# Kernel optimization log

Hardware: AMD Instinct MI355X
Metric: run time of the kernel (lower is better)

Reference implementation:

```python
import jax, jax.numpy as jnp
import numpy as np

S = 128           # inp_spatial_size
B = 4             # batch (4th coord column)
N = 200000        # active voxels
PLANES = (4, 8, 16, 32)   # feat_aug_mode='power', m=4
LEAK = 0.01
EPS = 1e-4        # sparseconvnet BatchNorm default eps
NOUT = 64


def _conv(x, w, stride, pad):
    return jax.lax.conv_general_dilated(
        x, w, (stride,) * 3, pad,
        dimension_numbers=('NCDHW', 'OIDHW', 'NCDHW'))


def _bn_lrelu(x, mask, g, b):
    # SCN BatchNormLeakyReLU: stats over ACTIVE sites only (x is zero at inactive)
    cnt = jnp.maximum(jnp.sum(mask), 1.0)
    mean = jnp.sum(x, axis=(0, 2, 3, 4)) / cnt
    var = jnp.sum(x * x, axis=(0, 2, 3, 4)) / cnt - mean * mean
    sc = (g * jax.lax.rsqrt(var + EPS))[None, :, None, None, None]
    y = (x - mean[None, :, None, None, None]) * sc + b[None, :, None, None, None]
    y = jnp.where(y >= 0, y, LEAK * y)
    return y * mask


def _pool2(x, red):
    b, c, d, h, w = x.shape
    return red(x.reshape(b, c, d // 2, 2, h // 2, 2, w // 2, 2), axis=(3, 5, 7))


def _forward(point_cloud, w0, g1, b1, wc1, g2, b2, wc2, g3, b3, wc3, wlin, blin):
    ci = point_cloud[:, :3].astype(jnp.int32)
    bi = point_cloud[:, 3].astype(jnp.int32)
    f = point_cloud[:, 4]
    # InputLayer mode=3: sum features of duplicate coordinates
    dense = jnp.zeros((B, 1, S, S, S), jnp.float32).at[bi, 0, ci[:, 0], ci[:, 1], ci[:, 2]].add(f)
    mask = jnp.zeros((B, 1, S, S, S), jnp.float32).at[bi, 0, ci[:, 0], ci[:, 1], ci[:, 2]].set(1.0)
    # SubmanifoldConvolution(3): dense 3^3 conv restricted to active output sites
    x = _conv(dense, w0, 1, 'SAME') * mask
    for g, b, wc in ((g1, b1, wc1), (g2, b2, wc2), (g3, b3, wc3)):
        x = _bn_lrelu(x, mask, g, b)
        x = _conv(x, wc, 2, 'VALID')        # sparse Convolution(k=2, s=2)
        mask = _pool2(mask, jnp.max)        # output active iff any input in window active
        x = x * mask
        x = _pool2(x, jnp.sum) / 8.0        # SCN AveragePooling(2,2): sum / poolVolume
        mask = _pool2(mask, jnp.max)
        x = x * mask
    # SparseToDense(32) + view(-1, D^3*C): row-major [B, C, D, D, D] flatten
    x = x.reshape(x.shape[0], -1)           # [B, 32*2^3] = [B, 256]
    return x @ wlin.T + blin                # use_linear_output -> [B, 64]


def setup_inputs() -> dict:
    key = jax.random.key(0)
    ks = jax.random.split(key, 10)
    coords = jax.random.randint(ks[0], (N, 3), 0, S).astype(jnp.float32)
    bidx = jax.random.randint(ks[1], (N, 1), 0, B).astype(jnp.float32)
    feats = jax.random.normal(ks[2], (N, 1), jnp.float32)
    point_cloud = jnp.concatenate([coords, bidx, feats], axis=1)

    def he(k, shape, fan_in):
        return jax.random.normal(k, shape, jnp.float32) / np.sqrt(fan_in)

    inp = {
        'point_cloud': point_cloud,
        'w0': he(ks[3], (PLANES[0], 1, 3, 3, 3), 27.0),
    }
    for i in range(3):
        cin, cout = PLANES[i], PLANES[i + 1]
        inp[f'g{i + 1}'] = jnp.ones((cin,), jnp.float32)
        inp[f'b{i + 1}'] = jnp.zeros((cin,), jnp.float32)
        inp[f'wc{i + 1}'] = he(ks[4 + i], (cout, cin, 2, 2, 2), cin * 8.0)
    d = S // 4 ** 3
    fan = PLANES[-1] * d ** 3
    inp['wlin'] = he(ks[8], (NOUT, fan), fan)
    inp['blin'] = jnp.zeros((NOUT,), jnp.float32)
    return inp


def reference(point_cloud, w0, g1, b1, wc1, g2, b2, wc2, g3, b3, wc3, wlin, blin):
    return _forward(point_cloud, w0, g1, b1, wc1, g2, b2, wc2, g3, b3, wc3, wlin, blin)
```

## Files before the change

kernel.cpp:

```cpp
#include <hip/hip_runtime.h>

#define SS 128
#define S3 (SS*SS*SS)
#define NBATCH 4
#define LEAK 0.01f
#define BNEPS 1e-4f
#define NTILE 16384
#define MAXSLOT 64

constexpr size_t OFF_DENSE    = 0;
constexpr size_t OFF_MASKBITS = OFF_DENSE + (size_t)NBATCH*S3*4;
constexpr size_t OFF_X1       = OFF_MASKBITS + (size_t)NBATCH*S3/8;
constexpr size_t OFF_MASK32   = OFF_X1 + (size_t)NBATCH*8*32768*4;
constexpr size_t OFF_MASK8    = OFF_MASK32 + (size_t)NBATCH*32768;
constexpr size_t OFF_STATS    = OFF_MASK8 + (size_t)NBATCH*512;
constexpr size_t OFF_P1       = OFF_STATS + 256;
constexpr size_t OFF_P2       = OFF_P1 + 256*9*4;
constexpr size_t OFF_P3       = OFF_P2 + 256*2*4;
constexpr size_t OFF_PM       = OFF_P3 + 64*2*4;
constexpr size_t OFF_NBLK     = OFF_PM + 16*4;
constexpr size_t OFF_LIST     = OFF_NBLK + NTILE*4;
constexpr size_t OFF_X0L      = OFF_LIST + (size_t)NTILE*MAXSLOT*4;
constexpr size_t OFF_X2       = OFF_X0L + (size_t)NTILE*MAXSLOT*16;
constexpr size_t OFF_X3       = OFF_X2 + (size_t)NBATCH*16*512*4;


__device__ inline float waveSum(float v) {
#pragma unroll
    for (int off = 32; off; off >>= 1) v += __shfl_xor(v, off, 64);
    return v;
}

__global__ void k_init(const float* __restrict__ pc, float* __restrict__ dense,
                       uint4* __restrict__ maskbits4, int n) {
    int blk = blockIdx.x;
    if (blk < 256) {
        maskbits4[blk * 256 + threadIdx.x] = make_uint4(0u, 0u, 0u, 0u);
        return;
    }
    int i = (blk - 256) * 256 + threadIdx.x;
    if (i >= n) return;
    int d = (int)pc[i*5+0], h = (int)pc[i*5+1], w = (int)pc[i*5+2], b = (int)pc[i*5+3];
    dense[(((size_t)b*SS + d)*SS + h)*SS + w] = 0.f;
}

__global__ void k_scatter(const float* __restrict__ pc, float* __restrict__ dense,
                          unsigned* __restrict__ maskbits, int n) {
    int i = blockIdx.x * blockDim.x + threadIdx.x;
    if (i >= n) return;
    float c0 = pc[i*5+0], c1 = pc[i*5+1], c2 = pc[i*5+2], cb = pc[i*5+3], f = pc[i*5+4];
    int d = (int)c0, h = (int)c1, w = (int)c2, b = (int)cb;
    unsigned vox = (((unsigned)b*SS + d)*SS + h)*SS + w;
    atomicAdd(&dense[vox], f);
    atomicOr(&maskbits[vox >> 5], 1u << (vox & 31));
}

__global__ __launch_bounds__(512) void k_conv0(const float* __restrict__ dense,
                                               const unsigned* __restrict__ maskbits,
                                               const float* __restrict__ w0g,
                                               unsigned* __restrict__ nblk,
                                               unsigned* __restrict__ list,
                                               float4* __restrict__ x0l,
                                               unsigned char* __restrict__ mask32) {
    __shared__ float lds[10*10*68];
    __shared__ float ws[108];
    __shared__ unsigned short wtot[8][8];
    __shared__ unsigned queue[8*MAXSLOT];
    __shared__ unsigned char cellocc[8][8];
    int tid = threadIdx.x;
    int lane = tid & 63, wid = tid >> 6;
    int th = blockIdx.x, td = blockIdx.y;
    int zb = blockIdx.z;
    int b = zb >> 1, wh = zb & 1;
    int d0 = td*8, h0 = th*8, w0 = wh*64;
    if (tid < 108) ws[tid] = w0g[tid];
    if (tid < 64) cellocc[tid>>3][tid&7] = 0;
    const float* dn = dense + (size_t)b * S3;
    for (int idx = tid; idx < 1600; idx += 512) {
        int r = idx >> 4, q = idx & 15;
        int dz = r / 10, dy = r - dz*10;
        int gz = d0 - 1 + dz, gy = h0 - 1 + dy;
        float4 v = make_float4(0.f, 0.f, 0.f, 0.f);
        if ((unsigned)gz < SS && (unsigned)gy < SS) {
            unsigned row = ((unsigned)b*SS + gz)*SS + gy;
            int gx = w0 + q*4;
            v = *(const float4*)(dn + ((size_t)gz*SS + gy)*SS + gx);
            unsigned mword = maskbits[row*4 + (gx >> 5)];
            int sh = gx & 31;
            if (!((mword >> (sh+0)) & 1u)) v.x = 0.f;
            if (!((mword >> (sh+1)) & 1u)) v.y = 0.f;
            if (!((mword >> (sh+2)) & 1u)) v.z = 0.f;
            if (!((mword >> (sh+3)) & 1u)) v.w = 0.f;
        }
        float* lrow = lds + r*68 + 1 + q*4;
        lrow[0]=v.x; lrow[1]=v.y; lrow[2]=v.z; lrow[3]=v.w;
    }
    for (int idx = tid; idx < 200; idx += 512) {
        int r = idx >> 1, side = idx & 1;
        int dz = r / 10, dy = r - dz*10;
        int gz = d0 - 1 + dz, gy = h0 - 1 + dy;
        int hgx = side ? (w0 + 64) : (w0 - 1);
        float hv = 0.f;
        if ((unsigned)gz < SS && (unsigned)gy < SS && (unsigned)hgx < SS) {
            unsigned row = ((unsigned)b*SS + gz)*SS + gy;
            float v = dn[((size_t)gz*SS + gy)*SS + hgx];
            unsigned mword = maskbits[row*4 + (hgx >> 5)];
            hv = ((mword >> (hgx & 31)) & 1u) ? v : 0.f;
        }
        lds[r*68 + (side ? 65 : 0)] = hv;
    }
    int tz = wid, ty = (tid >> 3) & 7, tx = tid & 7;
    int gz = d0 + tz, gy = h0 + ty;
    uint4 rb = ((const uint4*)maskbits)[((unsigned)b*SS + gz)*SS + gy];
    unsigned loW = wh ? rb.z : rb.x;
    unsigned hiW = wh ? rb.w : rb.y;
    unsigned occ8 = 0;
#pragma unroll
    for (int s=0;s<8;++s) {
        unsigned word = (s < 4) ? loW : hiW;
        occ8 |= (((word >> (((s&3)<<3) + tx)) & 1u) << s);
    }
    unsigned long long ballArr[8];
#pragma unroll
    for (int s=0;s<8;++s) {
        ballArr[s] = __ballot((occ8 >> s) & 1u);
        if (lane == 0) wtot[s][wid] = (unsigned short)__popcll(ballArr[s]);
    }
    __syncthreads();
    unsigned long long lmask = (1ull << lane) - 1ull;
    int blkbase = ((b*16 + td)*16 + th)*16 + wh*8;
    unsigned qb = 0;
#pragma unroll
    for (int s=0;s<8;++s) {
        unsigned base = 0, total = 0;
#pragma unroll
        for (int j=0;j<8;++j) { unsigned t = wtot[s][j]; if (j < wid) base += t; total += t; }
        unsigned tc = total < MAXSLOT ? total : MAXSLOT;
        if ((occ8 >> s) & 1u) {
            unsigned slot = base + (unsigned)__popcll(ballArr[s] & lmask);
            if (slot < MAXSLOT) queue[qb + slot] = (unsigned)tid | (s<<9) | (slot<<13);
            cellocc[s][((tz>>2)<<2) | ((ty>>2)<<1) | (tx>>2)] = 1;
        }
        qb += tc;
    }
    if (tid < 8) {
        unsigned total = 0;
#pragma unroll
        for (int j=0;j<8;++j) total += wtot[tid][j];
        nblk[blkbase + tid] = total < MAXSLOT ? total : MAXSLOT;
    }
    __syncthreads();
    if (tid < 64) {
        int s = tid >> 3, c = tid & 7;
        int cz = (c>>2)&1, cy = (c>>1)&1, cx = c&1;
        mask32[b*32768 + ((d0>>2)+cz)*1024 + ((h0>>2)+cy)*32 + wh*16 + s*2+cx] = cellocc[s][c];
    }
    for (unsigned i = tid; i < qb; i += 512) {
        unsigned e = queue[i];
        int et = e & 511, es = (e>>9) & 15, eslot = e >> 13;
        int ez = et >> 6, ey = (et>>3) & 7, ex = et & 7;
        int egx = es*8 + ex;
        float a0=0.f, a1=0.f, a2=0.f, a3=0.f;
#pragma unroll
        for (int kd=0; kd<3; ++kd)
#pragma unroll
            for (int kh=0; kh<3; ++kh)
#pragma unroll
                for (int kw=0; kw<3; ++kw) {
                    float v = lds[((ez+kd)*10 + ey+kh)*68 + egx + kw];
                    int kk = kd*9 + kh*3 + kw;
                    a0 += v*ws[kk]; a1 += v*ws[27+kk]; a2 += v*ws[54+kk]; a3 += v*ws[81+kk];
                }
        int blk = blkbase + es;
        unsigned vox = (((unsigned)b*SS + d0+ez)*SS + h0+ey)*SS + (w0 + egx);
        list[(size_t)blk*MAXSLOT + eslot] = vox;
        x0l[(size_t)blk*MAXSLOT + eslot] = make_float4(a0, a1, a2, a3);
    }
}

__global__ void k_stats1m(const float4* __restrict__ x0l, const unsigned* __restrict__ nblk,
                          const unsigned char* __restrict__ mask32, unsigned char* __restrict__ mask8,
                          float* __restrict__ p1, float* __restrict__ pm) {
    int tid = threadIdx.x;
    int bid = blockIdx.x;
    if (bid < 256) {
        __shared__ float red[4][9];
        int tid0 = bid * 256 + tid;
        float a[9] = {0,0,0,0,0,0,0,0,0};
        for (int s = tid0; s < NTILE*MAXSLOT; s += 65536) {
            int blk = s >> 6, sl = s & 63;
            if (sl < (int)nblk[blk]) {
                float4 v = x0l[s];
                a[0]+=v.x; a[1]+=v.y; a[2]+=v.z; a[3]+=v.w;
                a[4]+=v.x*v.x; a[5]+=v.y*v.y; a[6]+=v.z*v.z; a[7]+=v.w*v.w;
                a[8]+=1.f;
            }
        }
#pragma unroll
        for (int k=0;k<9;++k) a[k] = waveSum(a[k]);
        int wid = tid>>6, lane = tid&63;
        if (lane < 9) red[wid][lane] = a[lane];
        __syncthreads();
        if (tid < 9) p1[bid*9+tid] = red[0][tid]+red[1][tid]+red[2][tid]+red[3][tid];
        return;
    }
    __shared__ float redm[4];
    int blk = bid - 256;
    float c = 0.f;
    if (blk < 8) {
        int i = blk*256 + tid;
        int b = i>>9, r = i&511;
        int d8 = r>>6, h8 = (r>>3)&7, w8 = r&7;
        const unsigned char* m = mask32 + b*32768;
        unsigned v = 0;
#pragma unroll
        for (int dz=0;dz<2;++dz)
#pragma unroll
            for (int dy=0;dy<2;++dy)
#pragma unroll
                for (int dx=0;dx<2;++dx)
                    v |= m[(2*d8+dz)*1024 + (2*h8+dy)*32 + (2*w8+dx)];
        mask8[i] = (unsigned char)v;
        c = (float)v;
    } else {
        const uint4* m4 = (const uint4*)mask32;
        int base = ((blk-8)*256 + tid)*4;
#pragma unroll
        for (int j=0;j<4;++j) {
            uint4 x = m4[base+j];
            c += (float)(__popc(x.x) + __popc(x.y) + __popc(x.z) + __popc(x.w));
        }
    }
    c = waveSum(c);
    if ((tid & 63) == 0) redm[tid>>6] = c;
    __syncthreads();
    if (tid == 0) pm[blk] = redm[0]+redm[1]+redm[2]+redm[3];
}

__global__ __launch_bounds__(256) void k_prep1(const float* __restrict__ p1,
        const float* __restrict__ pm, const float* __restrict__ g1,
        const float* __restrict__ b1, float* __restrict__ stats) {
    __shared__ float red[4][9];
    __shared__ float tot[9];
    int tid = threadIdx.x;
    int wid = tid>>6, lane = tid&63;
    float a[9];
#pragma unroll
    for (int k=0;k<9;++k) a[k] = p1[tid*9+k];
#pragma unroll
    for (int k=0;k<9;++k) a[k] = waveSum(a[k]);
    if (lane < 9) red[wid][lane] = a[lane];
    __syncthreads();
    if (tid < 9) tot[tid] = red[0][tid]+red[1][tid]+red[2][tid]+red[3][tid];
    __syncthreads();
    if (tid < 4) {
        float cnt = fmaxf(tot[8], 1.f);
        float mean = tot[tid] / cnt;
        float var  = tot[4+tid] / cnt - mean*mean;
        float s = g1[tid] * rsqrtf(var + BNEPS);
        stats[2+tid] = s; stats[6+tid] = b1[tid] - mean*s;
    }
    if (tid == 4) { float s=0.f; for (int j=8;j<16;++j) s += pm[j]; stats[0] = s; }
    if (tid == 5) { float s=0.f; for (int j=0;j<8;++j)  s += pm[j]; stats[1] = s; }
}

__global__ void k_stage1(const float4* __restrict__ x0l, const unsigned* __restrict__ list,
                         const unsigned* __restrict__ nblk, const float* __restrict__ wc1,
                         const float* __restrict__ stats, float* __restrict__ x1) {
    __shared__ float acc[256];
    __shared__ float wsh[256];
    __shared__ float sc[4], sh[4];
    int tid = threadIdx.x;
    wsh[tid] = wc1[tid];
    acc[tid] = 0.f;
    if (tid < 4) { sc[tid] = stats[2+tid]; sh[tid] = stats[6+tid]; }
    __syncthreads();
    int s = blockIdx.x * 256 + tid;
    int blk = s >> 6, sl = s & 63;
    int lt = tid >> 6;
    if (sl < (int)nblk[blk]) {
        unsigned vox = list[s];
        float4 v = x0l[s];
        int w = vox & 127, h = (vox>>7)&127, d = (vox>>14)&127;
        float y[4];
        float t0 = v.x*sc[0]+sh[0]; y[0] = t0 >= 0.f ? t0 : LEAK*t0;
        float t1 = v.y*sc[1]+sh[1]; y[1] = t1 >= 0.f ? t1 : LEAK*t1;
        float t2 = v.z*sc[2]+sh[2]; y[2] = t2 >= 0.f ? t2 : LEAK*t2;
        float t3 = v.w*sc[3]+sh[3]; y[3] = t3 >= 0.f ? t3 : LEAK*t3;
        int widx = (d&1)*4 + (h&1)*2 + (w&1);
        int cell = ((d>>2)&1)*4 + ((h>>2)&1)*2 + ((w>>2)&1);
        float* ap = acc + lt*64 + cell;
#pragma unroll
        for (int o=0;o<8;++o) {
            const float* wp = wsh + o*32 + widx;
            float contrib = y[0]*wp[0] + y[1]*wp[8] + y[2]*wp[16] + y[3]*wp[24];
            atomicAdd(ap + o*8, contrib * 0.125f);
        }
    }
    __syncthreads();
    int rem = tid & 63, o = rem >> 3, cell = rem & 7;
    int blk2 = blockIdx.x*4 + (tid >> 6);
    int ss = blk2 & 15, th = (blk2>>4)&15, td = (blk2>>8)&15, b = blk2>>12;
    int cz = (cell>>2)&1, cy = (cell>>1)&1, cx = cell&1;
    x1[(size_t)b*8*32768 + o*32768 + (td*2+cz)*1024 + (th*2+cy)*32 + ss*2+cx] = acc[tid];
}

__global__ void k_s2stats(const float4* __restrict__ x1v, float* __restrict__ p2) {
    __shared__ float red[4][2];
    int blk = blockIdx.x;
    int plane = blk >> 3, chunk = blk & 7;
    const float4* p = x1v + (size_t)plane*8192 + chunk*1024;
    float s=0.f, sq=0.f;
    for (int i = threadIdx.x; i < 1024; i += 256) {
        float4 v = p[i];
        s  += v.x+v.y+v.z+v.w;
        sq += v.x*v.x+v.y*v.y+v.z*v.z+v.w*v.w;
    }
    s = waveSum(s); sq = waveSum(sq);
    int wid = threadIdx.x>>6, lane = threadIdx.x&63;
    if (lane == 0) { red[wid][0] = s; red[wid][1] = sq; }
    __syncthreads();
    if (threadIdx.x < 2)
        p2[blk*2+threadIdx.x] = red[0][threadIdx.x]+red[1][threadIdx.x]+red[2][threadIdx.x]+red[3][threadIdx.x];
}

__global__ void k_prep2(const float* __restrict__ p2, const float* __restrict__ g2,
                        const float* __restrict__ b2, float* __restrict__ stats) {
    __shared__ float sm[16];
    int tid = threadIdx.x;
    if (tid < 16) {
        int c = tid & 7, q = tid >> 3;
        float s = 0.f;
        for (int b=0;b<4;++b)
            for (int ch=0;ch<8;++ch)
                s += p2[((b*8+c)*8+ch)*2 + q];
        sm[tid] = s;
    }
    __syncthreads();
    if (tid < 8) {
        float cnt = fmaxf(stats[0], 1.f);
        float mean = sm[tid] / cnt;
        float var  = sm[8+tid] / cnt - mean*mean;
        float s = g2[tid] * rsqrtf(var + BNEPS);
        stats[10+tid] = s; stats[18+tid] = b2[tid] - mean*s;
    }
}

__global__ void k_stage2(const float* __restrict__ x1, const unsigned char* __restrict__ mask32,
                         const float* __restrict__ wc2, const float* __restrict__ stats,
                         float* __restrict__ x2) {
    int t = blockIdx.x * 4 + (threadIdx.x >> 6);
    int lane = threadIdx.x & 63;
    int r = t & 511, bo = t >> 9;
    int o = bo & 15, b = bo >> 4;
    int d8 = r >> 6, h8 = (r >> 3) & 7, w8 = r & 7;
    int dd = lane >> 4, hh = (lane >> 2) & 3, ww = lane & 3;
    int s32 = ((d8*4+dd) << 10) + ((h8*4+hh) << 5) + (w8*4+ww);
    const float* xb = x1 + (size_t)b*8*32768;
    float wreg = wc2[o*64 + lane];
    float m = mask32[b*32768 + s32] ? 1.f : 0.f;
    int widx = (dd&1)*4 + (hh&1)*2 + (ww&1);
    float acc = 0.f;
#pragma unroll
    for (int c=0;c<8;++c) {
        float v = xb[c*32768 + s32];
        float tt = v*stats[10+c] + stats[18+c];
        tt = (tt >= 0.f) ? tt : LEAK*tt;
        acc += tt * __shfl(wreg, c*8 + widx, 64);
    }
    acc = waveSum(acc * m);
    if (lane == 0) x2[t] = acc * 0.125f;
}

__global__ void k_s3stats(const float* __restrict__ x2, float* __restrict__ p3) {
    __shared__ float red[4][2];
    const float* p = x2 + (size_t)blockIdx.x * 512;
    float s=0.f, sq=0.f;
    for (int i = threadIdx.x; i < 512; i += 256) { float v = p[i]; s += v; sq += v*v; }
    s = waveSum(s); sq = waveSum(sq);
    int wid = threadIdx.x>>6, lane = threadIdx.x&63;
    if (lane == 0) { red[wid][0] = s; red[wid][1] = sq; }
    __syncthreads();
    if (threadIdx.x < 2)
        p3[blockIdx.x*2+threadIdx.x] = red[0][threadIdx.x]+red[1][threadIdx.x]+red[2][threadIdx.x]+red[3][threadIdx.x];
}

__global__ void k_prep3(const float* __restrict__ p3, const float* __restrict__ g3,
                        const float* __restrict__ b3, float* __restrict__ stats) {
    __shared__ float sm[32];
    int tid = threadIdx.x;
    if (tid < 32) {
        int c = tid & 15, q = tid >> 4;
        float s = 0.f;
        for (int b=0;b<4;++b) s += p3[(b*16+c)*2 + q];
        sm[tid] = s;
    }
    __syncthreads();
    if (tid < 16) {
        float cnt = fmaxf(stats[1], 1.f);
        float mean = sm[tid] / cnt;
        float var  = sm[16+tid] / cnt - mean*mean;
        float s = g3[tid] * rsqrtf(var + BNEPS);
        stats[26+tid] = s; stats[42+tid] = b3[tid] - mean*s;
    }
}

__global__ void k_stage3(const float* __restrict__ x2, const unsigned char* __restrict__ mask8,
                         const float* __restrict__ wc3, const float* __restrict__ stats,
                         float* __restrict__ x3) {
    int t = blockIdx.x * 4 + (threadIdx.x >> 6);
    int lane = threadIdx.x & 63;
    int r = t & 7, bo = t >> 3;
    int o = bo & 31, b = bo >> 5;
    int d2 = (r >> 2) & 1, h2 = (r >> 1) & 1, w2 = r & 1;
    int dd = lane >> 4, hh = (lane >> 2) & 3, ww = lane & 3;
    int s8 = (d2*4+dd)*64 + (h2*4+hh)*8 + (w2*4+ww);
    const float* xb = x2 + (size_t)b*16*512;
    float w0r = wc3[o*128 + lane];
    float w1r = wc3[o*128 + 64 + lane];
    float m = mask8[b*512 + s8] ? 1.f : 0.f;
    int widx = (dd&1)*4 + (hh&1)*2 + (ww&1);
    float acc = 0.f;
#pragma unroll
    for (int c=0;c<8;++c) {
        float v = xb[c*512 + s8];
        float tt = v*stats[26+c] + stats[42+c];
        tt = (tt >= 0.f) ? tt : LEAK*tt;
        acc += tt * __shfl(w0r, c*8 + widx, 64);
    }
#pragma unroll
    for (int c=8;c<16;++c) {
        float v = xb[c*512 + s8];
        float tt = v*stats[26+c] + stats[42+c];
        tt = (tt >= 0.f) ? tt : LEAK*tt;
        acc += tt * __shfl(w1r, (c-8)*8 + widx, 64);
    }
    acc = waveSum(acc * m);
    if (lane == 0) x3[t] = acc * 0.125f;
}

__global__ void k_linear(const float* __restrict__ x3, const float* __restrict__ wlin,
                         const float* __restrict__ blin, float* __restrict__ out) {
    int t = blockIdx.x * 4 + (threadIdx.x >> 6);
    int lane = threadIdx.x & 63;
    int b = t >> 6, j = t & 63;
    const float* xb = x3 + b*256;
    const float* wj = wlin + j*256;
    float acc = 0.f;
#pragma unroll
    for (int k=0;k<4;++k) acc += xb[k*64+lane] * wj[k*64+lane];
    acc = waveSum(acc);
    if (lane == 0) out[t] = acc + blin[j];
}

extern "C" void kernel_launch(void* const* d_in, const int* in_sizes, int n_in,
                              void* d_out, int out_size, void* d_ws, size_t ws_size,
                              hipStream_t stream) {
    const float* pc   = (const float*)d_in[0];
    const float* w0   = (const float*)d_in[1];
    const float* g1   = (const float*)d_in[2];
    const float* b1   = (const float*)d_in[3];
    const float* wc1  = (const float*)d_in[4];
    const float* g2   = (const float*)d_in[5];
    const float* b2   = (const float*)d_in[6];
    const float* wc2  = (const float*)d_in[7];
    const float* g3   = (const float*)d_in[8];
    const float* b3   = (const float*)d_in[9];
    const float* wc3  = (const float*)d_in[10];
    const float* wlin = (const float*)d_in[11];
    const float* blin = (const float*)d_in[12];
    float* out = (float*)d_out;

    char* ws = (char*)d_ws;
    float*         dense    = (float*)(ws + OFF_DENSE);
    unsigned*      maskbits = (unsigned*)(ws + OFF_MASKBITS);
    float*         x1       = (float*)(ws + OFF_X1);
    unsigned char* mask32   = (unsigned char*)(ws + OFF_MASK32);
    unsigned char* mask8    = (unsigned char*)(ws + OFF_MASK8);
    float*         stats    = (float*)(ws + OFF_STATS);
    float*         p1       = (float*)(ws + OFF_P1);
    float*         p2       = (float*)(ws + OFF_P2);
    float*         p3       = (float*)(ws + OFF_P3);
    float*         pm       = (float*)(ws + OFF_PM);
    unsigned*      nblk     = (unsigned*)(ws + OFF_NBLK);
    unsigned*      list     = (unsigned*)(ws + OFF_LIST);
    float4*        x0l      = (float4*)(ws + OFF_X0L);
    float*         x2       = (float*)(ws + OFF_X2);
    float*         x3       = (float*)(ws + OFF_X3);

    int n = in_sizes[0] / 5;
    int nb = (n + 255) / 256;

    k_init<<<256 + nb, 256, 0, stream>>>(pc, dense, (uint4*)maskbits, n);
    k_scatter<<<nb, 256, 0, stream>>>(pc, dense, maskbits, n);
    k_conv0<<<dim3(16,16,8), 512, 0, stream>>>(dense, maskbits, w0, nblk, list, x0l, mask32);
    k_stats1m<<<272, 256, 0, stream>>>(x0l, nblk, mask32, mask8, p1, pm);
    k_prep1<<<1, 256, 0, stream>>>(p1, pm, g1, b1, stats);
    k_stage1<<<NTILE/4, 256, 0, stream>>>(x0l, list, nblk, wc1, stats, x1);
    k_s2stats<<<256, 256, 0, stream>>>((const float4*)x1, p2);
    k_prep2<<<1, 64, 0, stream>>>(p2, g2, b2, stats);
    k_stage2<<<8192, 256, 0, stream>>>(x1, mask32, wc2, stats, x2);
    k_s3stats<<<64, 256, 0, stream>>>(x2, p3);
    k_prep3<<<1, 64, 0, stream>>>(p3, g3, b3, stats);
    k_stage3<<<256, 256, 0, stream>>>(x2, mask8, wc3, stats, x3);
    k_linear<<<64, 256, 0, stream>>>(x3, wlin, blin, out);
}
```

Measured before the change: 102.5 us.

## Restructure stage2 so one block computes all output channels per region

Stage 2 is reorganized so each block handles one (batch, 8^3 region) and computes all 16 output channels. The block stages the BN+LeakyReLU-transformed input tile (8 channels x 64 cells) and the full weight tensor in LDS. Before, each wave handled one output channel and re-read the same x1 inputs 16 times. Input reads now use float4 loads, and the reduction shrinks to a 16-lane shuffle. In exchange it adds LDS traffic and barriers, and launches 4x fewer blocks.

```diff
diff --git a/kernel.cpp b/kernel.cpp
--- a/kernel.cpp
+++ b/kernel.cpp
@@ -346,30 +346,57 @@
     }
 }
 
-__global__ void k_stage2(const float* __restrict__ x1, const unsigned char* __restrict__ mask32,
+__global__ __launch_bounds__(256) void k_stage2(const float* __restrict__ x1,
+                         const unsigned char* __restrict__ mask32,
                          const float* __restrict__ wc2, const float* __restrict__ stats,
                          float* __restrict__ x2) {
-    int t = blockIdx.x * 4 + (threadIdx.x >> 6);
-    int lane = threadIdx.x & 63;
-    int r = t & 511, bo = t >> 9;
-    int o = bo & 15, b = bo >> 4;
+    __shared__ float wsh[1024];
+    __shared__ float xin[8][64];
+    __shared__ float mLDS[64];
+    __shared__ float scs[8], shs[8];
+    int tid = threadIdx.x;
+    int br = blockIdx.x;
+    int b = br >> 9, r = br & 511;
     int d8 = r >> 6, h8 = (r >> 3) & 7, w8 = r & 7;
-    int dd = lane >> 4, hh = (lane >> 2) & 3, ww = lane & 3;
-    int s32 = ((d8*4+dd) << 10) + ((h8*4+hh) << 5) + (w8*4+ww);
-    const float* xb = x1 + (size_t)b*8*32768;
-    float wreg = wc2[o*64 + lane];
-    float m = mask32[b*32768 + s32] ? 1.f : 0.f;
-    int widx = (dd&1)*4 + (hh&1)*2 + (ww&1);
+    for (int i = tid; i < 1024; i += 256) wsh[i] = wc2[i];
+    if (tid < 8) { scs[tid] = stats[10+tid]; shs[tid] = stats[18+tid]; }
+    const unsigned char* mb = mask32 + b*32768;
+    if (tid < 64) {
+        int dd = tid >> 4, hh = (tid >> 2) & 3, ww = tid & 3;
+        mLDS[tid] = mb[(d8*4+dd)*1024 + (h8*4+hh)*32 + (w8*4+ww)] ? 1.f : 0.f;
+    }
+    __syncthreads();
+    if (tid < 128) {
+        int c = tid >> 4, f = tid & 15;
+        int dd = f >> 2, hh = f & 3;
+        const float* src = x1 + (size_t)b*8*32768 + c*32768
+                         + (d8*4+dd)*1024 + (h8*4+hh)*32 + w8*4;
+        float4 v = *(const float4*)src;
+        float sc = scs[c], sh = shs[c];
+        int cbase = dd*16 + hh*4;
+        float t0 = v.x*sc+sh; t0 = (t0>=0.f)?t0:LEAK*t0; xin[c][cbase+0] = t0 * mLDS[cbase+0];
+        float t1 = v.y*sc+sh; t1 = (t1>=0.f)?t1:LEAK*t1; xin[c][cbase+1] = t1 * mLDS[cbase+1];
+        float t2 = v.z*sc+sh; t2 = (t2>=0.f)?t2:LEAK*t2; xin[c][cbase+2] = t2 * mLDS[cbase+2];
+        float t3 = v.w*sc+sh; t3 = (t3>=0.f)?t3:LEAK*t3; xin[c][cbase+3] = t3 * mLDS[cbase+3];
+    }
+    __syncthreads();
+    int o = tid >> 4, g = tid & 15;
     float acc = 0.f;
 #pragma unroll
-    for (int c=0;c<8;++c) {
-        float v = xb[c*32768 + s32];
-        float tt = v*stats[10+c] + stats[18+c];
-        tt = (tt >= 0.f) ? tt : LEAK*tt;
-        acc += tt * __shfl(wreg, c*8 + widx, 64);
-    }
-    acc = waveSum(acc * m);
-    if (lane == 0) x2[t] = acc * 0.125f;
+    for (int j=0;j<4;++j) {
+        int cell = g*4 + j;
+        int dd = cell >> 4, hh = (cell >> 2) & 3, ww = cell & 3;
+        int widx = (dd&1)*4 + (hh&1)*2 + (ww&1);
+        const float* wp = wsh + o*64 + widx;
+#pragma unroll
+        for (int c=0;c<8;++c)
+            acc += xin[c][cell] * wp[c*8];
+    }
+    acc += __shfl_xor(acc, 1, 64);
+    acc += __shfl_xor(acc, 2, 64);
+    acc += __shfl_xor(acc, 4, 64);
+    acc += __shfl_xor(acc, 8, 64);
+    if (g == 0) x2[((size_t)b*16 + o)*512 + r] = acc * 0.125f;
 }
 
 __global__ void k_s3stats(const float* __restrict__ x2, float* __restrict__ p3) {
@@ -499,7 +526,7 @@
     k_stage1<<<NTILE/4, 256, 0, stream>>>(x0l, list, nblk, wc1, stats, x1);
     k_s2stats<<<256, 256, 0, stream>>>((const float4*)x1, p2);
     k_prep2<<<1, 64, 0, stream>>>(p2, g2, b2, stats);
-    k_stage2<<<8192, 256, 0, stream>>>(x1, mask32, wc2, stats, x2);
+    k_stage2<<<2048, 256, 0, stream>>>(x1, mask32, wc2, stats, x2);
     k_s3stats<<<64, 256, 0, stream>>>(x2, p3);
     k_prep3<<<1, 64, 0, stream>>>(p3, g3, b3, stats);
     k_stage3<<<256, 256, 0, stream>>>(x2, mask8, wc3, stats, x3);
```

Result: faster. 100.4 us, median of 2 (-2.1%).
